# Kernel tuning notes

Hardware: AMD Instinct MI355X
Metric: run time of the kernel (lower is better)

## Reference

```python
import jax, jax.numpy as jnp
import numpy as np

B, D, O, E, K = 8192, 2048, 2048, 8, 2


def setup_inputs() -> dict:
    key = jax.random.key(0)
    k1, k2, k3, k4 = jax.random.split(key, 4)
    x = jax.random.normal(k1, (B, D), dtype=jnp.float32)
    # router: Linear(D -> E)
    router_w = jax.random.normal(k2, (E, D), dtype=jnp.float32) * (1.0 / np.sqrt(D))
    router_b = jnp.zeros((E,), dtype=jnp.float32)
    # experts: [E, O, D] weight (xavier-uniform-like scale), [E, O] bias (zeros)
    lim = np.sqrt(6.0 / (D + O))
    expert_w = jax.random.uniform(k3, (E, O, D), dtype=jnp.float32, minval=-lim, maxval=lim)
    expert_b = jnp.zeros((E, O), dtype=jnp.float32)
    return {"x": x, "router_w": router_w, "router_b": router_b,
            "expert_w": expert_w, "expert_b": expert_b}


def reference(x, router_w, router_b, expert_w, expert_b):
    # router logits [B, E]
    logits = x @ router_w.T + router_b
    top_vals, top_idx = jax.lax.top_k(logits, K)          # [B, K]
    routing_weights = jax.nn.softmax(top_vals, axis=-1)   # softmax over top-k logits
    # dense per-(token, expert) combine weight [B, E]; zero for unselected experts
    onehot = jax.nn.one_hot(top_idx, E, dtype=x.dtype)    # [B, K, E]
    w_be = jnp.einsum('bk,bke->be', routing_weights, onehot)
    # per-expert linear, weighted combine (loop over small fixed E)
    out = jnp.zeros((x.shape[0], O), dtype=x.dtype)
    for e in range(E):
        out = out + w_be[:, e:e + 1] * (x @ expert_w[e].T + expert_b[e])
    return out
```

## Files before the change

### kernel.cpp

```cpp
#include <hip/hip_runtime.h>
#include <stdint.h>

#define NB 8192
#define ND 2048
#define NO 2048
#define NE 8

typedef __bf16 bf16x8 __attribute__((ext_vector_type(8)));
typedef float floatx4 __attribute__((ext_vector_type(4)));

__device__ __forceinline__ unsigned short f2bf(float f) {
    union { float f; uint32_t u; } v; v.f = f;
    uint32_t u = v.u;
    return (unsigned short)((u + 0x7FFFu + ((u >> 16) & 1u)) >> 16);
}

__global__ __launch_bounds__(256) void cvt2_bf16_kernel(
        const float* __restrict__ a, unsigned short* __restrict__ oa, int na4,
        const float* __restrict__ b, unsigned short* __restrict__ ob, int nb4) {
    int i = blockIdx.x * blockDim.x + threadIdx.x;
    int stride = gridDim.x * blockDim.x;
    int tot = na4 + nb4;
    for (; i < tot; i += stride) {
        const float4* src = (i < na4) ? (const float4*)a : (const float4*)b;
        ushort4* dst = (i < na4) ? (ushort4*)oa : (ushort4*)ob;
        int j = (i < na4) ? i : i - na4;
        float4 v = src[j];
        ushort4 o;
        o.x = f2bf(v.x); o.y = f2bf(v.y); o.z = f2bf(v.z); o.w = f2bf(v.w);
        dst[j] = o;
    }
}

__global__ __launch_bounds__(256) void router_topk_kernel(const float* __restrict__ x,
        const float* __restrict__ rw, const float* __restrict__ rb,
        int* __restrict__ i0a, int* __restrict__ i1a,
        float* __restrict__ w0a, float* __restrict__ w1a) {
    const int wave = threadIdx.x >> 6;
    const int lane = threadIdx.x & 63;
    const int t = blockIdx.x * 4 + wave;
    const float4* xp = (const float4*)(x + (size_t)t * ND);
    const float4* rp = (const float4*)rw;
    float acc[NE];
#pragma unroll
    for (int e = 0; e < NE; e++) acc[e] = 0.f;
#pragma unroll
    for (int i = 0; i < ND / 256; i++) {
        int idx = i * 64 + lane;
        float4 xv = xp[idx];
#pragma unroll
        for (int e = 0; e < NE; e++) {
            float4 rv = rp[(size_t)e * (ND / 4) + idx];
            acc[e] += xv.x * rv.x + xv.y * rv.y + xv.z * rv.z + xv.w * rv.w;
        }
    }
#pragma unroll
    for (int e = 0; e < NE; e++) {
        float v = acc[e];
#pragma unroll
        for (int s = 32; s > 0; s >>= 1) v += __shfl_xor(v, s, 64);
        acc[e] = v;
    }
    if (lane == 0) {
        float lg[NE];
#pragma unroll
        for (int e = 0; e < NE; e++) lg[e] = acc[e] + rb[e];
        int i0 = 0; float v0 = lg[0];
#pragma unroll
        for (int e = 1; e < NE; e++) if (lg[e] > v0) { v0 = lg[e]; i0 = e; }
        int i1 = -1; float v1 = -3.4e38f;
#pragma unroll
        for (int e = 0; e < NE; e++) if (e != i0 && lg[e] > v1) { v1 = lg[e]; i1 = e; }
        float ex = expf(v1 - v0);
        float inv = 1.f / (1.f + ex);
        i0a[t] = i0; i1a[t] = i1;
        w0a[t] = inv; w1a[t] = ex * inv;
    }
}

__global__ __launch_bounds__(256) void compact_kernel(
        const int* __restrict__ i0a, const int* __restrict__ i1a,
        const float* __restrict__ w0a, const float* __restrict__ w1a,
        int* __restrict__ cntA, int* __restrict__ cntB,
        int* __restrict__ tokA, float* __restrict__ wA,
        int* __restrict__ tokB, float* __restrict__ wB) {
    const int lane = threadIdx.x & 63;
    const int gw = (blockIdx.x * 256 + threadIdx.x) >> 6;
    const int t = gw * 64 + lane;
#pragma unroll
    for (int which = 0; which < 2; which++) {
        int sel   = which ? i1a[t] : i0a[t];
        float w   = which ? w1a[t] : w0a[t];
        int* cnt  = which ? cntB : cntA;
        int* tok  = which ? tokB : tokA;
        float* wl = which ? wB : wA;
        unsigned long long m[NE];
#pragma unroll
        for (int e = 0; e < NE; e++) m[e] = __ballot(sel == e);
        int slot = __popcll(m[sel] & ((1ull << lane) - 1ull));
        int base = 0;
        if (lane < NE) base = atomicAdd(&cnt[lane], (int)__popcll(m[lane]));
        base = __shfl(base, sel, 64);
        tok[sel * NB + base + slot] = t;
        wl[sel * NB + base + slot]  = w;
    }
}

#define GLL16(g, l) __builtin_amdgcn_global_load_lds( \
    (const __attribute__((address_space(1))) void*)(g), \
    (__attribute__((address_space(3))) void*)(l), 16, 0, 0)

template <bool ACCUM>
__global__ __launch_bounds__(256, 4) void moe_gemm_kernel(
        const unsigned short* __restrict__ xbf, const unsigned short* __restrict__ wbf,
        const float* __restrict__ eb, const int* __restrict__ cntArr,
        const int* __restrict__ listTok, const float* __restrict__ listW,
        float* __restrict__ out) {
    __shared__ unsigned short sA[128 * 32];
    __shared__ unsigned short sB[128 * 32];
    __shared__ int sTok[128];
    __shared__ float sW[128];

    const int e = blockIdx.z, mt = blockIdx.y, nt = blockIdx.x;
    const int cnt = cntArr[e];
    if (mt * 128 >= cnt) return;
    const int tid = threadIdx.x;
    if (tid < 128) {
        int r = mt * 128 + tid;
        bool ok = r < cnt;
        sTok[tid] = ok ? listTok[e * NB + r] : 0;
        sW[tid]   = ok ? listW[e * NB + r] : 0.f;
    }
    __syncthreads();

    const char* gA[2]; const char* gB[2];
    unsigned short* lA[2]; unsigned short* lB[2];
#pragma unroll
    for (int r = 0; r < 2; r++) {
        int c = r * 256 + tid;
        int row = c >> 2, colb = (c & 3) * 16;
        gA[r] = (const char*)xbf + (size_t)sTok[row] * (ND * 2) + colb;
        gB[r] = (const char*)wbf + ((size_t)e * NO + (size_t)nt * 128 + row) * (ND * 2) + colb;
        lA[r] = sA + c * 8;
        lB[r] = sB + c * 8;
    }

    const int wave = tid >> 6, lane = tid & 63;
    const int wm = (wave >> 1) * 64, wn = (wave & 1) * 64;
    const int lr = lane & 15, lq = lane >> 4;

    floatx4 acc[4][4];
#pragma unroll
    for (int mi = 0; mi < 4; mi++)
#pragma unroll
        for (int nj = 0; nj < 4; nj++) acc[mi][nj] = (floatx4){0.f, 0.f, 0.f, 0.f};

    for (int kk = 0; kk < ND / 32; kk++) {
#pragma unroll
        for (int r = 0; r < 2; r++) {
            GLL16(gA[r], lA[r]);
            GLL16(gB[r], lB[r]);
            gA[r] += 64; gB[r] += 64;
        }
        __syncthreads();
        bf16x8 af[4], bfr[4];
#pragma unroll
        for (int mi = 0; mi < 4; mi++)
            af[mi] = *(const bf16x8*)&sA[(wm + mi * 16 + lr) * 32 + lq * 8];
#pragma unroll
        for (int nj = 0; nj < 4; nj++)
            bfr[nj] = *(const bf16x8*)&sB[(wn + nj * 16 + lr) * 32 + lq * 8];
#pragma unroll
        for (int mi = 0; mi < 4; mi++)
#pragma unroll
            for (int nj = 0; nj < 4; nj++)
                acc[mi][nj] = __builtin_amdgcn_mfma_f32_16x16x32_bf16(af[mi], bfr[nj], acc[mi][nj], 0, 0, 0);
        __syncthreads();
    }

#pragma unroll
    for (int nj = 0; nj < 4; nj++) {
        int gn = nt * 128 + wn + nj * 16 + lr;
        float bias = eb[(size_t)e * NO + gn];
#pragma unroll
        for (int mi = 0; mi < 4; mi++) {
#pragma unroll
            for (int r = 0; r < 4; r++) {
                int m = wm + mi * 16 + lq * 4 + r;
                if (mt * 128 + m < cnt) {
                    float* p = out + (size_t)sTok[m] * NO + gn;
                    float v = sW[m] * (acc[mi][nj][r] + bias);
                    if (ACCUM) v += *p;
                    *p = v;
                }
            }
        }
    }
}

extern "C" void kernel_launch(void* const* d_in, const int* in_sizes, int n_in,
                              void* d_out, int out_size, void* d_ws, size_t ws_size,
                              hipStream_t stream) {
    const float* x        = (const float*)d_in[0];
    const float* router_w = (const float*)d_in[1];
    const float* router_b = (const float*)d_in[2];
    const float* expert_w = (const float*)d_in[3];
    const float* expert_b = (const float*)d_in[4];
    float* out = (float*)d_out;
    char* ws = (char*)d_ws;

    unsigned short* xbf = (unsigned short*)ws;
    unsigned short* wbf = (unsigned short*)(ws + 33554432);
    size_t o = 100663296;
    int*   tokA = (int*)(ws + o);   o += NE * NB * 4;
    float* wA   = (float*)(ws + o); o += NE * NB * 4;
    int*   tokB = (int*)(ws + o);   o += NE * NB * 4;
    float* wB   = (float*)(ws + o); o += NE * NB * 4;
    int*   i0a  = (int*)(ws + o);   o += NB * 4;
    int*   i1a  = (int*)(ws + o);   o += NB * 4;
    float* w0a  = (float*)(ws + o); o += NB * 4;
    float* w1a  = (float*)(ws + o); o += NB * 4;
    int*   cntA = (int*)(ws + o);   o += 128;
    int*   cntB = (int*)(ws + o);   o += 128;

    hipMemsetAsync(cntA, 0, 256, stream);
    cvt2_bf16_kernel<<<2048, 256, 0, stream>>>(x, xbf, NB * ND / 4,
                                               expert_w, wbf, NE * NO * ND / 4);
    router_topk_kernel<<<NB / 4, 256, 0, stream>>>(x, router_w, router_b, i0a, i1a, w0a, w1a);
    compact_kernel<<<NB / 64 / 4, 256, 0, stream>>>(i0a, i1a, w0a, w1a,
                                                    cntA, cntB, tokA, wA, tokB, wB);
    moe_gemm_kernel<false><<<dim3(NO / 128, NB / 128, NE), 256, 0, stream>>>(
        xbf, wbf, expert_b, cntA, tokA, wA, out);
    moe_gemm_kernel<true><<<dim3(NO / 128, NB / 128, NE), 256, 0, stream>>>(
        xbf, wbf, expert_b, cntB, tokB, wB, out);
}
```

Before: 603.8 us.

## Triple-buffer MoE GEMM K-loop, merge expert passes with atomics, fuse x conversion

Result: faster. 591.4 us (-2.1%).

```diff
diff --git a/kernel.cpp b/kernel.cpp
--- a/kernel.cpp
+++ b/kernel.cpp
@@ -5,6 +5,7 @@
 #define ND 2048
 #define NO 2048
 #define NE 8
+#define NT (ND / 32)
 
 typedef __bf16 bf16x8 __attribute__((ext_vector_type(8)));
 typedef float floatx4 __attribute__((ext_vector_type(4)));
@@ -15,25 +16,21 @@
     return (unsigned short)((u + 0x7FFFu + ((u >> 16) & 1u)) >> 16);
 }
 
-__global__ __launch_bounds__(256) void cvt2_bf16_kernel(
-        const float* __restrict__ a, unsigned short* __restrict__ oa, int na4,
-        const float* __restrict__ b, unsigned short* __restrict__ ob, int nb4) {
+__global__ __launch_bounds__(256) void cvt_bf16_kernel(
+        const float* __restrict__ b, unsigned short* __restrict__ ob, int n4) {
     int i = blockIdx.x * blockDim.x + threadIdx.x;
     int stride = gridDim.x * blockDim.x;
-    int tot = na4 + nb4;
-    for (; i < tot; i += stride) {
-        const float4* src = (i < na4) ? (const float4*)a : (const float4*)b;
-        ushort4* dst = (i < na4) ? (ushort4*)oa : (ushort4*)ob;
-        int j = (i < na4) ? i : i - na4;
-        float4 v = src[j];
+    for (; i < n4; i += stride) {
+        float4 v = ((const float4*)b)[i];
         ushort4 o;
         o.x = f2bf(v.x); o.y = f2bf(v.y); o.z = f2bf(v.z); o.w = f2bf(v.w);
-        dst[j] = o;
+        ((ushort4*)ob)[i] = o;
     }
 }
 
 __global__ __launch_bounds__(256) void router_topk_kernel(const float* __restrict__ x,
         const float* __restrict__ rw, const float* __restrict__ rb,
+        unsigned short* __restrict__ xbf,
         int* __restrict__ i0a, int* __restrict__ i1a,
         float* __restrict__ w0a, float* __restrict__ w1a) {
     const int wave = threadIdx.x >> 6;
@@ -41,6 +38,7 @@
     const int t = blockIdx.x * 4 + wave;
     const float4* xp = (const float4*)(x + (size_t)t * ND);
     const float4* rp = (const float4*)rw;
+    ushort4* xo = (ushort4*)(xbf + (size_t)t * ND);
     float acc[NE];
 #pragma unroll
     for (int e = 0; e < NE; e++) acc[e] = 0.f;
@@ -48,6 +46,9 @@
     for (int i = 0; i < ND / 256; i++) {
         int idx = i * 64 + lane;
         float4 xv = xp[idx];
+        ushort4 o;
+        o.x = f2bf(xv.x); o.y = f2bf(xv.y); o.z = f2bf(xv.z); o.w = f2bf(xv.w);
+        xo[idx] = o;
 #pragma unroll
         for (int e = 0; e < NE; e++) {
             float4 rv = rp[(size_t)e * (ND / 4) + idx];
@@ -81,9 +82,7 @@
 __global__ __launch_bounds__(256) void compact_kernel(
         const int* __restrict__ i0a, const int* __restrict__ i1a,
         const float* __restrict__ w0a, const float* __restrict__ w1a,
-        int* __restrict__ cntA, int* __restrict__ cntB,
-        int* __restrict__ tokA, float* __restrict__ wA,
-        int* __restrict__ tokB, float* __restrict__ wB) {
+        int* __restrict__ cnt, int* __restrict__ tok, float* __restrict__ wl) {
     const int lane = threadIdx.x & 63;
     const int gw = (blockIdx.x * 256 + threadIdx.x) >> 6;
     const int t = gw * 64 + lane;
@@ -91,9 +90,6 @@
     for (int which = 0; which < 2; which++) {
         int sel   = which ? i1a[t] : i0a[t];
         float w   = which ? w1a[t] : w0a[t];
-        int* cnt  = which ? cntB : cntA;
-        int* tok  = which ? tokB : tokA;
-        float* wl = which ? wB : wA;
         unsigned long long m[NE];
 #pragma unroll
         for (int e = 0; e < NE; e++) m[e] = __ballot(sel == e);
@@ -110,14 +106,13 @@
     (const __attribute__((address_space(1))) void*)(g), \
     (__attribute__((address_space(3))) void*)(l), 16, 0, 0)
 
-template <bool ACCUM>
-__global__ __launch_bounds__(256, 4) void moe_gemm_kernel(
+__global__ __launch_bounds__(256, 3) void moe_gemm_kernel(
         const unsigned short* __restrict__ xbf, const unsigned short* __restrict__ wbf,
         const float* __restrict__ eb, const int* __restrict__ cntArr,
         const int* __restrict__ listTok, const float* __restrict__ listW,
         float* __restrict__ out) {
-    __shared__ unsigned short sA[128 * 32];
-    __shared__ unsigned short sB[128 * 32];
+    __shared__ unsigned short sA[3][128 * 32];
+    __shared__ unsigned short sB[3][128 * 32];
     __shared__ int sTok[128];
     __shared__ float sW[128];
 
@@ -134,20 +129,25 @@
     __syncthreads();
 
     const char* gA[2]; const char* gB[2];
-    unsigned short* lA[2]; unsigned short* lB[2];
+    int offAB[2];
 #pragma unroll
     for (int r = 0; r < 2; r++) {
         int c = r * 256 + tid;
         int row = c >> 2, colb = (c & 3) * 16;
         gA[r] = (const char*)xbf + (size_t)sTok[row] * (ND * 2) + colb;
         gB[r] = (const char*)wbf + ((size_t)e * NO + (size_t)nt * 128 + row) * (ND * 2) + colb;
-        lA[r] = sA + c * 8;
-        lB[r] = sB + c * 8;
+        offAB[r] = c * 16;
     }
 
     const int wave = tid >> 6, lane = tid & 63;
     const int wm = (wave >> 1) * 64, wn = (wave & 1) * 64;
     const int lr = lane & 15, lq = lane >> 4;
+    int roA[4], roB[4];
+#pragma unroll
+    for (int i = 0; i < 4; i++) {
+        roA[i] = (wm + i * 16 + lr) * 32 + lq * 8;
+        roB[i] = (wn + i * 16 + lr) * 32 + lq * 8;
+    }
 
     floatx4 acc[4][4];
 #pragma unroll
@@ -155,27 +155,54 @@
 #pragma unroll
         for (int nj = 0; nj < 4; nj++) acc[mi][nj] = (floatx4){0.f, 0.f, 0.f, 0.f};
 
-    for (int kk = 0; kk < ND / 32; kk++) {
-#pragma unroll
-        for (int r = 0; r < 2; r++) {
-            GLL16(gA[r], lA[r]);
-            GLL16(gB[r], lB[r]);
-            gA[r] += 64; gB[r] += 64;
+#pragma unroll
+    for (int r = 0; r < 2; r++) {
+        GLL16(gA[r], (char*)sA[0] + offAB[r]);
+        GLL16(gB[r], (char*)sB[0] + offAB[r]);
+        gA[r] += 64; gB[r] += 64;
+    }
+#pragma unroll
+    for (int r = 0; r < 2; r++) {
+        GLL16(gA[r], (char*)sA[1] + offAB[r]);
+        GLL16(gB[r], (char*)sB[1] + offAB[r]);
+        gA[r] += 64; gB[r] += 64;
+    }
+
+    int cur = 0;
+#pragma unroll 1
+    for (int t = 0; t < NT; t++) {
+        int nxt = cur + 2; if (nxt >= 3) nxt -= 3;
+        if (t + 2 < NT) {
+#pragma unroll
+            for (int r = 0; r < 2; r++) {
+                GLL16(gA[r], (char*)sA[nxt] + offAB[r]);
+                GLL16(gB[r], (char*)sB[nxt] + offAB[r]);
+                gA[r] += 64; gB[r] += 64;
+            }
+            asm volatile("s_waitcnt vmcnt(8)" ::: "memory");
+        } else if (t + 2 == NT) {
+            asm volatile("s_waitcnt vmcnt(4)" ::: "memory");
+        } else {
+            asm volatile("s_waitcnt vmcnt(0)" ::: "memory");
         }
-        __syncthreads();
+        __builtin_amdgcn_s_barrier();
+
+        const unsigned short* sAc = sA[cur];
+        const unsigned short* sBc = sB[cur];
         bf16x8 af[4], bfr[4];
 #pragma unroll
-        for (int mi = 0; mi < 4; mi++)
-            af[mi] = *(const bf16x8*)&sA[(wm + mi * 16 + lr) * 32 + lq * 8];
-#pragma unroll
-        for (int nj = 0; nj < 4; nj++)
-            bfr[nj] = *(const bf16x8*)&sB[(wn + nj * 16 + lr) * 32 + lq * 8];
+        for (int mi = 0; mi < 4; mi++) af[mi] = *(const bf16x8*)&sAc[roA[mi]];
+#pragma unroll
+        for (int nj = 0; nj < 4; nj++) bfr[nj] = *(const bf16x8*)&sBc[roB[nj]];
 #pragma unroll
         for (int mi = 0; mi < 4; mi++)
 #pragma unroll
             for (int nj = 0; nj < 4; nj++)
                 acc[mi][nj] = __builtin_amdgcn_mfma_f32_16x16x32_bf16(af[mi], bfr[nj], acc[mi][nj], 0, 0, 0);
-        __syncthreads();
+
+        asm volatile("s_waitcnt lgkmcnt(0)" ::: "memory");
+        __builtin_amdgcn_s_barrier();
+        cur = cur + 1 == 3 ? 0 : cur + 1;
     }
 
 #pragma unroll
@@ -188,10 +215,8 @@
             for (int r = 0; r < 4; r++) {
                 int m = wm + mi * 16 + lq * 4 + r;
                 if (mt * 128 + m < cnt) {
-                    float* p = out + (size_t)sTok[m] * NO + gn;
-                    float v = sW[m] * (acc[mi][nj][r] + bias);
-                    if (ACCUM) v += *p;
-                    *p = v;
+                    atomicAdd(out + (size_t)sTok[m] * NO + gn,
+                              sW[m] * (acc[mi][nj][r] + bias));
                 }
             }
         }
@@ -212,25 +237,20 @@
     unsigned short* xbf = (unsigned short*)ws;
     unsigned short* wbf = (unsigned short*)(ws + 33554432);
     size_t o = 100663296;
-    int*   tokA = (int*)(ws + o);   o += NE * NB * 4;
-    float* wA   = (float*)(ws + o); o += NE * NB * 4;
-    int*   tokB = (int*)(ws + o);   o += NE * NB * 4;
-    float* wB   = (float*)(ws + o); o += NE * NB * 4;
+    int*   tokL = (int*)(ws + o);   o += NE * NB * 4;
+    float* wL   = (float*)(ws + o); o += NE * NB * 4;
     int*   i0a  = (int*)(ws + o);   o += NB * 4;
     int*   i1a  = (int*)(ws + o);   o += NB * 4;
     float* w0a  = (float*)(ws + o); o += NB * 4;
     float* w1a  = (float*)(ws + o); o += NB * 4;
-    int*   cntA = (int*)(ws + o);   o += 128;
-    int*   cntB = (int*)(ws + o);   o += 128;
-
-    hipMemsetAsync(cntA, 0, 256, stream);
-    cvt2_bf16_kernel<<<2048, 256, 0, stream>>>(x, xbf, NB * ND / 4,
-                                               expert_w, wbf, NE * NO * ND / 4);
-    router_topk_kernel<<<NB / 4, 256, 0, stream>>>(x, router_w, router_b, i0a, i1a, w0a, w1a);
-    compact_kernel<<<NB / 64 / 4, 256, 0, stream>>>(i0a, i1a, w0a, w1a,
-                                                    cntA, cntB, tokA, wA, tokB, wB);
-    moe_gemm_kernel<false><<<dim3(NO / 128, NB / 128, NE), 256, 0, stream>>>(
-        xbf, wbf, expert_b, cntA, tokA, wA, out);
-    moe_gemm_kernel<true><<<dim3(NO / 128, NB / 128, NE), 256, 0, stream>>>(
-        xbf, wbf, expert_b, cntB, tokB, wB, out);
-}
+    int*   cnt  = (int*)(ws + o);   o += 128;
+
+    hipMemsetAsync(cnt, 0, 128, stream);
+    hipMemsetAsync(out, 0, (size_t)NB * NO * 4, stream);
+    router_topk_kernel<<<NB / 4, 256, 0, stream>>>(x, router_w, router_b, xbf,
+                                                   i0a, i1a, w0a, w1a);
+    cvt_bf16_kernel<<<2048, 256, 0, stream>>>(expert_w, wbf, NE * NO * ND / 4);
+    compact_kernel<<<NB / 64 / 4, 256, 0, stream>>>(i0a, i1a, w0a, w1a, cnt, tokL, wL);
+    moe_gemm_kernel<<<dim3(NO / 128, NB / 128, NE), 256, 0, stream>>>(
+        xbf, wbf, expert_b, cnt, tokL, wL, out);
+}
```
